# Performance work log

Hardware: AMD Instinct MI355X
Metric: run time of the kernel (lower is better)

Reference implementation:

```python
import jax, jax.numpy as jnp
import numpy as np

B, S, D, H = 2, 2048, 768, 12
DK = D // H

def setup_inputs() -> dict:
    key = jax.random.key(0)
    ks = jax.random.split(key, 8)
    query = jax.random.normal(ks[0], (B, S, D), dtype=jnp.float32)
    key_t = jax.random.normal(ks[1], (B, S, D), dtype=jnp.float32)
    value = jax.random.normal(ks[2], (B, S, D), dtype=jnp.float32)
    # causal (look-ahead) mask: True above the diagonal -> masked
    mask = jnp.triu(jnp.ones((S, S), dtype=bool), k=1)[None, None]  # (1,1,S,S)
    scale = 1.0 / np.sqrt(D)
    w_q = jax.random.normal(ks[3], (D, D), dtype=jnp.float32) * scale
    w_k = jax.random.normal(ks[4], (D, D), dtype=jnp.float32) * scale
    w_v = jax.random.normal(ks[5], (D, D), dtype=jnp.float32) * scale
    w_o = jax.random.normal(ks[6], (D, D), dtype=jnp.float32) * scale
    return {"query": query, "key": key_t, "value": value, "mask": mask,
            "w_q": w_q, "w_k": w_k, "w_v": w_v, "w_o": w_o}

def reference(query, key, value, mask, w_q, w_k, w_v, w_o):
    b = query.shape[0]
    # nn.Linear(bias=False): y = x @ W.T
    q = (query @ w_q.T).reshape(b, -1, H, DK).transpose(0, 2, 1, 3)  # (B,H,Sq,dk)
    k = (key @ w_k.T).reshape(b, -1, H, DK).transpose(0, 2, 1, 3)    # (B,H,Sk,dk)
    v = (value @ w_v.T).reshape(b, -1, H, DK).transpose(0, 2, 1, 3)  # (B,H,Sk,dk)
    scores = jnp.einsum('bhqd,bhkd->bhqk', q, k) / jnp.sqrt(jnp.float32(DK))
    scores = jnp.where(mask, jnp.float32(-1e9), scores)
    attn_weights = jax.nn.softmax(scores, axis=-1)  # (B,H,Sq,Sk); dropout=0 (eval)
    context = jnp.einsum('bhqk,bhkd->bhqd', attn_weights, v)
    context = context.transpose(0, 2, 1, 3).reshape(b, -1, D)
    output = context @ w_o.T
    return output, attn_weights
```

## Files before the change

### kernel.cpp

```cpp
#include <hip/hip_runtime.h>

#define BATCH 2
#define S_LEN 2048
#define NH 12
#define DMODEL 768

#define N8_BSD (BATCH * S_LEN * DMODEL / 8)
#define N8_DD (DMODEL * DMODEL / 8)

typedef __attribute__((ext_vector_type(8))) short bf16x8;
typedef __attribute__((ext_vector_type(4))) float f32x4;
typedef __attribute__((ext_vector_type(4))) unsigned short us4;

__device__ __forceinline__ unsigned short f2bf(float f) {
  union { float f; unsigned int u; } v; v.f = f;
  unsigned int r = v.u + 0x7fffu + ((v.u >> 16) & 1u);
  return (unsigned short)(r >> 16);
}

__global__ void cvt3_kernel(const float* __restrict__ s0,
                            const float* __restrict__ s1,
                            const float* __restrict__ s2,
                            unsigned short* __restrict__ dst,
                            float* __restrict__ ctx1) {
  int i = blockIdx.x * blockDim.x + threadIdx.x;
  int j = i / N8_BSD;
  int k = i - j * N8_BSD;
  const float* s = (j == 0) ? s0 : (j == 1) ? s1 : s2;
  const float4* sp = (const float4*)s;
  float4 a = sp[k * 2], b = sp[k * 2 + 1];
  us4 o0 = { f2bf(a.x), f2bf(a.y), f2bf(a.z), f2bf(a.w) };
  us4 o1 = { f2bf(b.x), f2bf(b.y), f2bf(b.z), f2bf(b.w) };
  us4* d = (us4*)dst;
  d[i * 2] = o0;
  d[i * 2 + 1] = o1;
  if (j == 0) {
    f32x4 z = (f32x4){0.f, 0.f, 0.f, 0.f};
    f32x4* c = (f32x4*)ctx1;
    c[k * 2] = z;
    c[k * 2 + 1] = z;
  }
}

__global__ void cvt4_kernel(const float* __restrict__ s0,
                            const float* __restrict__ s1,
                            const float* __restrict__ s2,
                            const float* __restrict__ s3,
                            unsigned short* __restrict__ dst) {
  int i = blockIdx.x * blockDim.x + threadIdx.x;
  int j = i / N8_DD;
  int k = i - j * N8_DD;
  const float* s = (j == 0) ? s0 : (j == 1) ? s1 : (j == 2) ? s2 : s3;
  const float4* sp = (const float4*)s;
  float4 a = sp[k * 2], b = sp[k * 2 + 1];
  us4 o0 = { f2bf(a.x), f2bf(a.y), f2bf(a.z), f2bf(a.w) };
  us4 o1 = { f2bf(b.x), f2bf(b.y), f2bf(b.z), f2bf(b.w) };
  us4* d = (us4*)dst;
  d[i * 2] = o0;
  d[i * 2 + 1] = o1;
}

__global__ void ctx_reduce(const float* __restrict__ c0,
                           const float* __restrict__ c1,
                           unsigned short* __restrict__ o) {
  int i = blockIdx.x * blockDim.x + threadIdx.x;
  float4 a = ((const float4*)c0)[i];
  float4 b = ((const float4*)c1)[i];
  us4 r = { f2bf(a.x + b.x), f2bf(a.y + b.y), f2bf(a.z + b.z), f2bf(a.w + b.w) };
  ((us4*)o)[i] = r;
}

#define GLD_LDS16(g, l)                                                    \
  __builtin_amdgcn_global_load_lds(                                        \
      (const __attribute__((address_space(1))) unsigned int*)(g),          \
      (__attribute__((address_space(3))) unsigned int*)(l), 16, 0, 0)

__global__ __launch_bounds__(256, 2)
void gemm_qkv(const unsigned short* __restrict__ Aq,
              const unsigned short* __restrict__ Ak,
              const unsigned short* __restrict__ Av,
              const unsigned short* __restrict__ W3,
              unsigned short* __restrict__ Qs,
              unsigned short* __restrict__ Ks,
              unsigned short* __restrict__ VT) {
  __shared__ unsigned short As[128 * 64];
  __shared__ unsigned short Bs[128 * 64];
  const int m0 = blockIdx.x * 128;
  const int n0g = blockIdx.y * 128;
  const int nblk = n0g / 768;
  const int n0 = n0g - nblk * 768;
  const unsigned short* A = (nblk == 0) ? Aq : (nblk == 1) ? Ak : Av;
  const unsigned short* Bw = W3 + (size_t)n0g * DMODEL;
  const int tid = threadIdx.x, w = tid >> 6, l = tid & 63;
  const int lg = l >> 4, ll = l & 15;
  const int wm = w >> 1, wn = w & 1;
  const int lr = l >> 3, lc = (l & 7) * 8;

  f32x4 acc[4][4];
#pragma unroll
  for (int i = 0; i < 4; ++i)
#pragma unroll
    for (int j = 0; j < 4; ++j) acc[i][j] = (f32x4){0.f, 0.f, 0.f, 0.f};

  for (int k0 = 0; k0 < DMODEL; k0 += 64) {
#pragma unroll
    for (int i = 0; i < 4; ++i) {
      GLD_LDS16(A + (size_t)(m0 + w * 32 + i * 8 + lr) * DMODEL + k0 + lc,
                &As[(w * 32 + i * 8) * 64]);
      GLD_LDS16(Bw + (size_t)(w * 32 + i * 8 + lr) * DMODEL + k0 + lc,
                &Bs[(w * 32 + i * 8) * 64]);
    }
    __syncthreads();
#pragma unroll
    for (int t = 0; t < 2; ++t) {
      bf16x8 af[4], bf[4];
#pragma unroll
      for (int mi = 0; mi < 4; ++mi)
        af[mi] = *(const bf16x8*)&As[(wm * 64 + mi * 16 + ll) * 64 + t * 32 + lg * 8];
#pragma unroll
      for (int ni = 0; ni < 4; ++ni)
        bf[ni] = *(const bf16x8*)&Bs[(wn * 64 + ni * 16 + ll) * 64 + t * 32 + lg * 8];
#pragma unroll
      for (int mi = 0; mi < 4; ++mi)
#pragma unroll
        for (int ni = 0; ni < 4; ++ni)
          acc[mi][ni] = __builtin_amdgcn_mfma_f32_16x16x32_bf16(
              af[mi], bf[ni], acc[mi][ni], 0, 0, 0);
    }
    __syncthreads();
  }

  if (nblk < 2) {
    unsigned short* o = nblk ? Ks : Qs;
    const float sc = nblk ? 1.f : 0.125f;
#pragma unroll
    for (int mi = 0; mi < 4; ++mi)
#pragma unroll
      for (int ni = 0; ni < 4; ++ni) {
        const int col = n0 + wn * 64 + ni * 16 + ll;
        const int rowb = m0 + wm * 64 + mi * 16 + lg * 4;
#pragma unroll
        for (int r = 0; r < 4; ++r)
          o[(size_t)(rowb + r) * 768 + col] = f2bf(acc[mi][ni][r] * sc);
      }
  } else {
#pragma unroll
    for (int mi = 0; mi < 4; ++mi)
#pragma unroll
      for (int ni = 0; ni < 4; ++ni) {
        const int col = n0 + wn * 64 + ni * 16 + ll;
        const int row = m0 + wm * 64 + mi * 16 + lg * 4;
        const int bb = row >> 11, sidx = row & (S_LEN - 1);
        const size_t base =
            ((size_t)(bb * NH + (col >> 6)) * 64 + (col & 63)) * S_LEN + sidx;
        us4 pk = { f2bf(acc[mi][ni][0]), f2bf(acc[mi][ni][1]),
                   f2bf(acc[mi][ni][2]), f2bf(acc[mi][ni][3]) };
        *(us4*)&VT[base] = pk;
      }
  }
}

__global__ __launch_bounds__(256, 2)
void gemm_proj(const unsigned short* __restrict__ A,
               const unsigned short* __restrict__ Bw,
               float* __restrict__ o) {
  __shared__ unsigned short As[128 * 64];
  __shared__ unsigned short Bs[128 * 64];
  const int m0 = blockIdx.x * 128, n0 = blockIdx.y * 128;
  const int tid = threadIdx.x, w = tid >> 6, l = tid & 63;
  const int lg = l >> 4, ll = l & 15;
  const int wm = w >> 1, wn = w & 1;
  const int lr = l >> 3, lc = (l & 7) * 8;

  f32x4 acc[4][4];
#pragma unroll
  for (int i = 0; i < 4; ++i)
#pragma unroll
    for (int j = 0; j < 4; ++j) acc[i][j] = (f32x4){0.f, 0.f, 0.f, 0.f};

  for (int k0 = 0; k0 < DMODEL; k0 += 64) {
#pragma unroll
    for (int i = 0; i < 4; ++i) {
      GLD_LDS16(A + (size_t)(m0 + w * 32 + i * 8 + lr) * DMODEL + k0 + lc,
                &As[(w * 32 + i * 8) * 64]);
      GLD_LDS16(Bw + (size_t)(n0 + w * 32 + i * 8 + lr) * DMODEL + k0 + lc,
                &Bs[(w * 32 + i * 8) * 64]);
    }
    __syncthreads();
#pragma unroll
    for (int t = 0; t < 2; ++t) {
      bf16x8 af[4], bf[4];
#pragma unroll
      for (int mi = 0; mi < 4; ++mi)
        af[mi] = *(const bf16x8*)&As[(wm * 64 + mi * 16 + ll) * 64 + t * 32 + lg * 8];
#pragma unroll
      for (int ni = 0; ni < 4; ++ni)
        bf[ni] = *(const bf16x8*)&Bs[(wn * 64 + ni * 16 + ll) * 64 + t * 32 + lg * 8];
#pragma unroll
      for (int mi = 0; mi < 4; ++mi)
#pragma unroll
        for (int ni = 0; ni < 4; ++ni)
          acc[mi][ni] = __builtin_amdgcn_mfma_f32_16x16x32_bf16(
              af[mi], bf[ni], acc[mi][ni], 0, 0, 0);
    }
    __syncthreads();
  }

#pragma unroll
  for (int mi = 0; mi < 4; ++mi)
#pragma unroll
    for (int ni = 0; ni < 4; ++ni) {
      const int col = n0 + wn * 64 + ni * 16 + ll;
      const int rowb = m0 + wm * 64 + mi * 16 + lg * 4;
#pragma unroll
      for (int r = 0; r < 4; ++r)
        o[(size_t)(rowb + r) * DMODEL + col] = acc[mi][ni][r];
    }
}

#define STAGE_TILE(srcTile, srcStride, ldsT)                                  \
  {                                                                           \
    _Pragma("unroll") for (int j_ = 0; j_ < 2; ++j_) {                        \
      int slot_ = (j_ * 4 + w) * 64 + l;                                      \
      int row_ = slot_ >> 3, c16_ = slot_ & 7;                                \
      GLD_LDS16((srcTile) + (size_t)row_ * (srcStride) +                      \
                    ((c16_ ^ (row_ & 7)) << 3),                               \
                (ldsT) + (j_ * 4 + w) * 512);                                 \
    }                                                                         \
  }

__global__ __launch_bounds__(256, 3)
void attn_ml(const unsigned short* __restrict__ Qp,
             const unsigned short* __restrict__ Kp,
             float2* __restrict__ mlbuf) {
  const int idx = blockIdx.x;
  const int qt = 31 - idx / (NH * BATCH);
  const int hb = idx % (NH * BATCH);
  const int h = hb >> 1, b = hb & 1;
  const int tid = threadIdx.x, w = tid >> 6, l = tid & 63;
  const int lg = l >> 4, ll = l & 15;
  __shared__ unsigned short Kt[2][64 * 64];

  const unsigned short* kbp = Kp + (size_t)b * S_LEN * DMODEL + h * 64;
  const int q0 = qt * 64 + w * 16;
  const int nkt = qt + 1;

  bf16x8 qf[2];
  {
    const unsigned short* qb =
        Qp + (size_t)(b * S_LEN + q0 + ll) * DMODEL + h * 64 + lg * 8;
    qf[0] = *(const bf16x8*)qb;
    qf[1] = *(const bf16x8*)(qb + 32);
  }
  int rowg[4];
#pragma unroll
  for (int r = 0; r < 4; ++r) rowg[r] = q0 + lg * 4 + r;

  float m[4], lsum[4];
#pragma unroll
  for (int r = 0; r < 4; ++r) { m[r] = -1e30f; lsum[r] = 0.f; }

  STAGE_TILE(kbp + (size_t)0 * 64 * DMODEL, DMODEL, &Kt[0][0]);
  __syncthreads();

  for (int kt = 0; kt < nkt; ++kt) {
    const int cur = kt & 1;
    if (kt + 1 < nkt)
      STAGE_TILE(kbp + (size_t)(kt + 1) * 64 * DMODEL, DMODEL, &Kt[cur ^ 1][0]);
    bf16x8 kf[8];
#pragma unroll
    for (int t = 0; t < 2; ++t)
#pragma unroll
      for (int nb = 0; nb < 4; ++nb) {
        const int row = nb * 16 + ll;
        kf[t * 4 + nb] = *(const bf16x8*)&Kt[cur][row * 64 +
            (((t * 4 + lg) ^ (row & 7)) << 3)];
      }
    f32x4 sv[4];
#pragma unroll
    for (int nb = 0; nb < 4; ++nb) sv[nb] = (f32x4){0.f, 0.f, 0.f, 0.f};
#pragma unroll
    for (int t = 0; t < 2; ++t)
#pragma unroll
      for (int nb = 0; nb < 4; ++nb)
        sv[nb] = __builtin_amdgcn_mfma_f32_16x16x32_bf16(qf[t], kf[t * 4 + nb],
                                                         sv[nb], 0, 0, 0);
    if (kt == nkt - 1) {
#pragma unroll
      for (int nb = 0; nb < 4; ++nb) {
        const int col = kt * 64 + nb * 16 + ll;
#pragma unroll
        for (int r = 0; r < 4; ++r)
          if (col > rowg[r]) sv[nb][r] = -1e30f;
      }
    }
#pragma unroll
    for (int r = 0; r < 4; ++r) {
      float tm = fmaxf(fmaxf(sv[0][r], sv[1][r]), fmaxf(sv[2][r], sv[3][r]));
      float mn = fmaxf(m[r], tm);
      float te = __expf(sv[0][r] - mn) + __expf(sv[1][r] - mn) +
                 __expf(sv[2][r] - mn) + __expf(sv[3][r] - mn);
      lsum[r] = lsum[r] * __expf(m[r] - mn) + te;
      m[r] = mn;
    }
    __syncthreads();
  }

#pragma unroll
  for (int off = 1; off < 16; off <<= 1)
#pragma unroll
    for (int r = 0; r < 4; ++r) {
      float om = __shfl_xor(m[r], off, 64);
      float ol = __shfl_xor(lsum[r], off, 64);
      float mn = fmaxf(m[r], om);
      lsum[r] = lsum[r] * __expf(m[r] - mn) + ol * __expf(om - mn);
      m[r] = mn;
    }

  if (ll == 0) {
    float2* mlb = mlbuf + (size_t)(b * NH + h) * S_LEN;
#pragma unroll
    for (int r = 0; r < 4; ++r)
      mlb[rowg[r]] = make_float2(m[r], 1.f / lsum[r]);
  }
}

__global__ __launch_bounds__(256, 3)
void attn_p2(const unsigned short* __restrict__ Qp,
             const unsigned short* __restrict__ Kp,
             const unsigned short* __restrict__ VTp,
             const float2* __restrict__ mlbuf,
             float* __restrict__ attnw,
             float* __restrict__ ctx0,
             float* __restrict__ ctx1) {
  const int idx = blockIdx.x;
  const int slot = idx / (NH * BATCH);
  const int hb = idx % (NH * BATCH);
  const int h = hb >> 1, b = hb & 1;
  int qt, ck;
  if (slot <= 16)      { ck = 0; qt = 15 + slot; }
  else if (slot == 17) { ck = 1; qt = 31; }
  else if (slot < 48)  { int u = slot - 18; int k = 15 - (u >> 1);
                         if (u & 1) { ck = 1; qt = k + 15; } else { ck = 0; qt = k - 1; } }
  else                 { ck = 1; qt = slot - 48; }

  const int ktlo = ck * 16;
  const int kthi = (qt < ktlo + 15) ? qt : (ktlo + 15);
  const bool hasval = (ktlo <= qt);

  const int tid = threadIdx.x, w = tid >> 6, l = tid & 63;
  const int lg = l >> 4, ll = l & 15;
  __shared__ unsigned short Kt[2][64 * 64];
  __shared__ unsigned short Vt[2][64 * 64];
  __shared__ float pf32[4][1024];
  float* pfw = &pf32[w][0];

  const unsigned short* kbp = Kp + (size_t)b * S_LEN * DMODEL + h * 64;
  const unsigned short* vbp = VTp + ((size_t)(b * NH + h)) * 64 * S_LEN;
  float* pbase = attnw + ((size_t)(b * NH + h)) * S_LEN * S_LEN;

  const int q0 = qt * 64 + w * 16;
  int rowg[4];
#pragma unroll
  for (int r = 0; r < 4; ++r) rowg[r] = q0 + lg * 4 + r;

  if (hasval) {
    bf16x8 qf[2];
    {
      const unsigned short* qb =
          Qp + (size_t)(b * S_LEN + q0 + ll) * DMODEL + h * 64 + lg * 8;
      qf[0] = *(const bf16x8*)qb;
      qf[1] = *(const bf16x8*)(qb + 32);
    }
    float m[4], linv[4];
    {
      const float2* mlb = mlbuf + (size_t)(b * NH + h) * S_LEN;
#pragma unroll
      for (int r = 0; r < 4; ++r) {
        float2 t = mlb[rowg[r]];
        m[r] = t.x;
        linv[r] = t.y;
      }
    }

    f32x4 cacc[4];
#pragma unroll
    for (int nb = 0; nb < 4; ++nb) cacc[nb] = (f32x4){0.f, 0.f, 0.f, 0.f};

    STAGE_TILE(kbp + (size_t)ktlo * 64 * DMODEL, DMODEL, &Kt[0][0]);
    STAGE_TILE(vbp + (size_t)ktlo * 64, S_LEN, &Vt[0][0]);
    __syncthreads();

    for (int kt = ktlo; kt <= kthi; ++kt) {
      const int cur = (kt - ktlo) & 1;
      if (kt < kthi) {
        STAGE_TILE(kbp + (size_t)(kt + 1) * 64 * DMODEL, DMODEL, &Kt[cur ^ 1][0]);
        STAGE_TILE(vbp + (size_t)(kt + 1) * 64, S_LEN, &Vt[cur ^ 1][0]);
      }
      bf16x8 kf[8];
#pragma unroll
      for (int t = 0; t < 2; ++t)
#pragma unroll
        for (int nb = 0; nb < 4; ++nb) {
          const int row = nb * 16 + ll;
          kf[t * 4 + nb] = *(const bf16x8*)&Kt[cur][row * 64 +
              (((t * 4 + lg) ^ (row & 7)) << 3)];
        }
      f32x4 sv[4];
#pragma unroll
      for (int nb = 0; nb < 4; ++nb) sv[nb] = (f32x4){0.f, 0.f, 0.f, 0.f};
#pragma unroll
      for (int t = 0; t < 2; ++t)
#pragma unroll
        for (int nb = 0; nb < 4; ++nb)
          sv[nb] = __builtin_amdgcn_mfma_f32_16x16x32_bf16(qf[t], kf[t * 4 + nb],
                                                           sv[nb], 0, 0, 0);
#pragma unroll
      for (int nb = 0; nb < 4; ++nb) {
        const int col = kt * 64 + nb * 16 + ll;
#pragma unroll
        for (int r = 0; r < 4; ++r) {
          float p = (col <= rowg[r]) ? __expf(sv[nb][r] - m[r]) * linv[r] : 0.f;
          const int rl = lg * 4 + r;
          pfw[rl * 64 + ((nb * 16 + ll) ^ ((lg & 1) << 4))] = p;
        }
      }
      bf16x8 pf[2];
#pragma unroll
      for (int t = 0; t < 2; ++t) {
        const int c0 = (t * 32 + lg * 8) ^ (((ll >> 2) & 1) << 4);
        f32x4 lo = *(const f32x4*)&pfw[ll * 64 + c0];
        f32x4 hi = *(const f32x4*)&pfw[ll * 64 + c0 + 4];
        union { us4 hh[2]; bf16x8 v; } u;
        u.hh[0] = (us4){ f2bf(lo[0]), f2bf(lo[1]), f2bf(lo[2]), f2bf(lo[3]) };
        u.hh[1] = (us4){ f2bf(hi[0]), f2bf(hi[1]), f2bf(hi[2]), f2bf(hi[3]) };
        pf[t] = u.v;
      }
      bf16x8 vf[8];
#pragma unroll
      for (int t = 0; t < 2; ++t)
#pragma unroll
        for (int nb = 0; nb < 4; ++nb) {
          const int row = nb * 16 + ll;
          vf[t * 4 + nb] = *(const bf16x8*)&Vt[cur][row * 64 +
              (((t * 4 + lg) ^ (row & 7)) << 3)];
        }
#pragma unroll
      for (int t = 0; t < 2; ++t)
#pragma unroll
        for (int nb = 0; nb < 4; ++nb)
          cacc[nb] = __builtin_amdgcn_mfma_f32_16x16x32_bf16(
              pf[t], vf[t * 4 + nb], cacc[nb], 0, 0, 0);
#pragma unroll
      for (int ps = 0; ps < 4; ++ps) {
        const int row = ps * 4 + lg;
        const int cb = (ll * 4) ^ ((ps & 1) << 4);
        f32x4 pv = *(const f32x4*)&pfw[row * 64 + cb];
        *(f32x4*)&pbase[(size_t)(q0 + row) * S_LEN + kt * 64 + ll * 4] = pv;
      }
      __syncthreads();
    }

#pragma unroll
    for (int nb = 0; nb < 4; ++nb)
#pragma unroll
      for (int r = 0; r < 4; ++r) {
        const int rl = lg * 4 + r;
        pfw[rl * 64 + ((nb * 16 + ll) ^ ((lg & 1) << 4))] = cacc[nb][r];
      }
    float* co = ck ? ctx1 : ctx0;
#pragma unroll
    for (int ps = 0; ps < 4; ++ps) {
      const int row = ps * 4 + lg;
      const int cb = (ll * 4) ^ ((ps & 1) << 4);
      f32x4 cv = *(const f32x4*)&pfw[row * 64 + cb];
      *(f32x4*)&co[(size_t)(b * S_LEN + q0 + row) * DMODEL + h * 64 + ll * 4] = cv;
    }
  }

  const int zs = ((qt + 1) * 64 > ktlo * 64) ? (qt + 1) * 64 : ktlo * 64;
  const int ze = (ktlo + 16) * 64;
  if (zs < ze) {
    f32x4 z = (f32x4){0.f, 0.f, 0.f, 0.f};
    for (int rr = 0; rr < 16; ++rr) {
      float* dst = pbase + (size_t)(q0 + rr) * S_LEN;
      for (int c = zs + l * 4; c < ze; c += 256)
        *(f32x4*)(dst + c) = z;
    }
  }
}

extern "C" void kernel_launch(void* const* d_in, const int* in_sizes, int n_in,
                              void* d_out, int out_size, void* d_ws, size_t ws_size,
                              hipStream_t stream) {
  const float* q_in = (const float*)d_in[0];
  const float* k_in = (const float*)d_in[1];
  const float* v_in = (const float*)d_in[2];
  const float* wq = (const float*)d_in[4];
  const float* wk = (const float*)d_in[5];
  const float* wv = (const float*)d_in[6];
  const float* wo = (const float*)d_in[7];

  const int BSD = BATCH * S_LEN * DMODEL;
  const int DD = DMODEL * DMODEL;
  const int M = BATCH * S_LEN;

  char* ws = (char*)d_ws;
  unsigned short* qbf = (unsigned short*)ws;  ws += (size_t)BSD * 2;
  unsigned short* kbf = (unsigned short*)ws;  ws += (size_t)BSD * 2;
  unsigned short* vbf = (unsigned short*)ws;  ws += (size_t)BSD * 2;
  unsigned short* wqb = (unsigned short*)ws;  ws += (size_t)DD * 2;
  unsigned short* wkb = (unsigned short*)ws;  ws += (size_t)DD * 2;
  unsigned short* wvb = (unsigned short*)ws;  ws += (size_t)DD * 2;
  unsigned short* wob = (unsigned short*)ws;  ws += (size_t)DD * 2;
  unsigned short* Qs  = (unsigned short*)ws;  ws += (size_t)BSD * 2;
  unsigned short* Ks  = (unsigned short*)ws;  ws += (size_t)BSD * 2;
  unsigned short* VT  = (unsigned short*)ws;  ws += (size_t)BSD * 2;
  unsigned short* ctx = (unsigned short*)ws;  ws += (size_t)BSD * 2;
  float* ctx0 = (float*)ws;                   ws += (size_t)BSD * 4;
  float* ctx1 = (float*)ws;                   ws += (size_t)BSD * 4;
  float2* mlbuf = (float2*)ws;                ws += (size_t)M * NH * sizeof(float2);
  (void)wkb; (void)wvb;

  float* out_proj = (float*)d_out;
  float* attnw = (float*)d_out + BSD;

  cvt3_kernel<<<3 * N8_BSD / 256, 256, 0, stream>>>(q_in, k_in, v_in, qbf, ctx1);
  cvt4_kernel<<<4 * N8_DD / 256, 256, 0, stream>>>(wq, wk, wv, wo, wqb);

  gemm_qkv<<<dim3(M / 128, 2304 / 128), 256, 0, stream>>>(qbf, kbf, vbf, wqb,
                                                          Qs, Ks, VT);

  attn_ml<<<32 * NH * BATCH, 256, 0, stream>>>(Qs, Ks, mlbuf);
  attn_p2<<<64 * NH * BATCH, 256, 0, stream>>>(Qs, Ks, VT, mlbuf, attnw,
                                               ctx0, ctx1);
  ctx_reduce<<<BSD / 4 / 256, 256, 0, stream>>>(ctx0, ctx1, ctx);

  gemm_proj<<<dim3(M / 128, DMODEL / 128), 256, 0, stream>>>(ctx, wob, out_proj);
}
```

Measured before the change: 218.4 us.

## Split attention pass-2 key tiles across warps with LDS cross-warp context reduction

Each warp now handles all 64 query rows of the tile for every fourth key tile, instead of each warp owning 16 query rows across all key tiles. K and V fragments are read straight from global memory rather than double-buffered through shared memory, which removes the per-tile __syncthreads. The four per-warp partial contexts are summed through shared memory at the end. This costs more registers (occupancy hint drops from 3 to 2), a larger per-warp LDS scratch, and uncached, uncoalesced-style global K/V reads. Blocks with few key tiles also leave some warps idle.

```diff
diff --git a/kernel.cpp b/kernel.cpp
--- a/kernel.cpp
+++ b/kernel.cpp
@@ -325,7 +325,7 @@
   }
 }
 
-__global__ __launch_bounds__(256, 3)
+__global__ __launch_bounds__(256, 2)
 void attn_p2(const unsigned short* __restrict__ Qp,
              const unsigned short* __restrict__ Kp,
              const unsigned short* __restrict__ VTp,
@@ -350,140 +350,149 @@
 
   const int tid = threadIdx.x, w = tid >> 6, l = tid & 63;
   const int lg = l >> 4, ll = l & 15;
-  __shared__ unsigned short Kt[2][64 * 64];
-  __shared__ unsigned short Vt[2][64 * 64];
-  __shared__ float pf32[4][1024];
+  __shared__ float pf32[4][64 * 64];
   float* pfw = &pf32[w][0];
 
   const unsigned short* kbp = Kp + (size_t)b * S_LEN * DMODEL + h * 64;
   const unsigned short* vbp = VTp + ((size_t)(b * NH + h)) * 64 * S_LEN;
   float* pbase = attnw + ((size_t)(b * NH + h)) * S_LEN * S_LEN;
-
-  const int q0 = qt * 64 + w * 16;
-  int rowg[4];
-#pragma unroll
-  for (int r = 0; r < 4; ++r) rowg[r] = q0 + lg * 4 + r;
+  const int q0g = qt * 64;
 
   if (hasval) {
-    bf16x8 qf[2];
-    {
+    bf16x8 qf[4][2];
+#pragma unroll
+    for (int rb = 0; rb < 4; ++rb) {
       const unsigned short* qb =
-          Qp + (size_t)(b * S_LEN + q0 + ll) * DMODEL + h * 64 + lg * 8;
-      qf[0] = *(const bf16x8*)qb;
-      qf[1] = *(const bf16x8*)(qb + 32);
-    }
-    float m[4], linv[4];
+          Qp + (size_t)(b * S_LEN + q0g + rb * 16 + ll) * DMODEL + h * 64 + lg * 8;
+      qf[rb][0] = *(const bf16x8*)qb;
+      qf[rb][1] = *(const bf16x8*)(qb + 32);
+    }
+    float m16[4][4], li16[4][4];
     {
       const float2* mlb = mlbuf + (size_t)(b * NH + h) * S_LEN;
 #pragma unroll
-      for (int r = 0; r < 4; ++r) {
-        float2 t = mlb[rowg[r]];
-        m[r] = t.x;
-        linv[r] = t.y;
-      }
-    }
-
-    f32x4 cacc[4];
-#pragma unroll
-    for (int nb = 0; nb < 4; ++nb) cacc[nb] = (f32x4){0.f, 0.f, 0.f, 0.f};
-
-    STAGE_TILE(kbp + (size_t)ktlo * 64 * DMODEL, DMODEL, &Kt[0][0]);
-    STAGE_TILE(vbp + (size_t)ktlo * 64, S_LEN, &Vt[0][0]);
-    __syncthreads();
-
-    for (int kt = ktlo; kt <= kthi; ++kt) {
-      const int cur = (kt - ktlo) & 1;
-      if (kt < kthi) {
-        STAGE_TILE(kbp + (size_t)(kt + 1) * 64 * DMODEL, DMODEL, &Kt[cur ^ 1][0]);
-        STAGE_TILE(vbp + (size_t)(kt + 1) * 64, S_LEN, &Vt[cur ^ 1][0]);
-      }
-      bf16x8 kf[8];
-#pragma unroll
-      for (int t = 0; t < 2; ++t)
-#pragma unroll
-        for (int nb = 0; nb < 4; ++nb) {
-          const int row = nb * 16 + ll;
-          kf[t * 4 + nb] = *(const bf16x8*)&Kt[cur][row * 64 +
-              (((t * 4 + lg) ^ (row & 7)) << 3)];
+      for (int rb = 0; rb < 4; ++rb)
+#pragma unroll
+        for (int r = 0; r < 4; ++r) {
+          float2 t = mlb[q0g + rb * 16 + lg * 4 + r];
+          m16[rb][r] = t.x;
+          li16[rb][r] = t.y;
         }
-      f32x4 sv[4];
-#pragma unroll
-      for (int nb = 0; nb < 4; ++nb) sv[nb] = (f32x4){0.f, 0.f, 0.f, 0.f};
-#pragma unroll
-      for (int t = 0; t < 2; ++t)
-#pragma unroll
-        for (int nb = 0; nb < 4; ++nb)
-          sv[nb] = __builtin_amdgcn_mfma_f32_16x16x32_bf16(qf[t], kf[t * 4 + nb],
-                                                           sv[nb], 0, 0, 0);
-#pragma unroll
-      for (int nb = 0; nb < 4; ++nb) {
-        const int col = kt * 64 + nb * 16 + ll;
-#pragma unroll
-        for (int r = 0; r < 4; ++r) {
-          float p = (col <= rowg[r]) ? __expf(sv[nb][r] - m[r]) * linv[r] : 0.f;
-          const int rl = lg * 4 + r;
-          pfw[rl * 64 + ((nb * 16 + ll) ^ ((lg & 1) << 4))] = p;
+    }
+
+    f32x4 cacc[4][4];
+#pragma unroll
+    for (int rb = 0; rb < 4; ++rb)
+#pragma unroll
+      for (int vb = 0; vb < 4; ++vb) cacc[rb][vb] = (f32x4){0.f, 0.f, 0.f, 0.f};
+
+    for (int kt = ktlo + w; kt <= kthi; kt += 4) {
+#pragma unroll
+      for (int hh = 0; hh < 2; ++hh) {
+        bf16x8 kf[2][2];
+#pragma unroll
+        for (int t = 0; t < 2; ++t)
+#pragma unroll
+          for (int nbl = 0; nbl < 2; ++nbl) {
+            const int nb = hh * 2 + nbl;
+            kf[t][nbl] = *(const bf16x8*)(kbp +
+                (size_t)(kt * 64 + nb * 16 + ll) * DMODEL + t * 32 + lg * 8);
+          }
+        f32x4 sv[4][2];
+#pragma unroll
+        for (int rb = 0; rb < 4; ++rb)
+#pragma unroll
+          for (int nbl = 0; nbl < 2; ++nbl) sv[rb][nbl] = (f32x4){0.f, 0.f, 0.f, 0.f};
+#pragma unroll
+        for (int t = 0; t < 2; ++t)
+#pragma unroll
+          for (int rb = 0; rb < 4; ++rb)
+#pragma unroll
+            for (int nbl = 0; nbl < 2; ++nbl)
+              sv[rb][nbl] = __builtin_amdgcn_mfma_f32_16x16x32_bf16(
+                  qf[rb][t], kf[t][nbl], sv[rb][nbl], 0, 0, 0);
+#pragma unroll
+        for (int nbl = 0; nbl < 2; ++nbl) {
+          const int nb = hh * 2 + nbl;
+          const int col = kt * 64 + nb * 16 + ll;
+#pragma unroll
+          for (int rb = 0; rb < 4; ++rb)
+#pragma unroll
+            for (int r = 0; r < 4; ++r) {
+              const int row = q0g + rb * 16 + lg * 4 + r;
+              float p = (col <= row)
+                            ? __expf(sv[rb][nbl][r] - m16[rb][r]) * li16[rb][r]
+                            : 0.f;
+              pfw[(rb * 16 + lg * 4 + r) * 64 +
+                  ((nb * 16 + ll) ^ ((lg & 1) << 4))] = p;
+            }
         }
       }
-      bf16x8 pf[2];
 #pragma unroll
       for (int t = 0; t < 2; ++t) {
-        const int c0 = (t * 32 + lg * 8) ^ (((ll >> 2) & 1) << 4);
-        f32x4 lo = *(const f32x4*)&pfw[ll * 64 + c0];
-        f32x4 hi = *(const f32x4*)&pfw[ll * 64 + c0 + 4];
-        union { us4 hh[2]; bf16x8 v; } u;
-        u.hh[0] = (us4){ f2bf(lo[0]), f2bf(lo[1]), f2bf(lo[2]), f2bf(lo[3]) };
-        u.hh[1] = (us4){ f2bf(hi[0]), f2bf(hi[1]), f2bf(hi[2]), f2bf(hi[3]) };
-        pf[t] = u.v;
-      }
-      bf16x8 vf[8];
-#pragma unroll
-      for (int t = 0; t < 2; ++t)
-#pragma unroll
-        for (int nb = 0; nb < 4; ++nb) {
-          const int row = nb * 16 + ll;
-          vf[t * 4 + nb] = *(const bf16x8*)&Vt[cur][row * 64 +
-              (((t * 4 + lg) ^ (row & 7)) << 3)];
+        bf16x8 pfr[4];
+#pragma unroll
+        for (int rb = 0; rb < 4; ++rb) {
+          const int row = rb * 16 + ll;
+          const int c0 = (t * 32 + lg * 8) ^ (((ll >> 2) & 1) << 4);
+          f32x4 lo = *(const f32x4*)&pfw[row * 64 + c0];
+          f32x4 hi = *(const f32x4*)&pfw[row * 64 + c0 + 4];
+          union { us4 hh2[2]; bf16x8 v; } u;
+          u.hh2[0] = (us4){ f2bf(lo[0]), f2bf(lo[1]), f2bf(lo[2]), f2bf(lo[3]) };
+          u.hh2[1] = (us4){ f2bf(hi[0]), f2bf(hi[1]), f2bf(hi[2]), f2bf(hi[3]) };
+          pfr[rb] = u.v;
         }
-#pragma unroll
-      for (int t = 0; t < 2; ++t)
-#pragma unroll
-        for (int nb = 0; nb < 4; ++nb)
-          cacc[nb] = __builtin_amdgcn_mfma_f32_16x16x32_bf16(
-              pf[t], vf[t * 4 + nb], cacc[nb], 0, 0, 0);
-#pragma unroll
-      for (int ps = 0; ps < 4; ++ps) {
+        bf16x8 vf[4];
+#pragma unroll
+        for (int vb = 0; vb < 4; ++vb)
+          vf[vb] = *(const bf16x8*)(vbp +
+              (size_t)(vb * 16 + ll) * S_LEN + kt * 64 + t * 32 + lg * 8);
+#pragma unroll
+        for (int rb = 0; rb < 4; ++rb)
+#pragma unroll
+          for (int vb = 0; vb < 4; ++vb)
+            cacc[rb][vb] = __builtin_amdgcn_mfma_f32_16x16x32_bf16(
+                pfr[rb], vf[vb], cacc[rb][vb], 0, 0, 0);
+      }
+#pragma unroll
+      for (int ps = 0; ps < 16; ++ps) {
         const int row = ps * 4 + lg;
         const int cb = (ll * 4) ^ ((ps & 1) << 4);
         f32x4 pv = *(const f32x4*)&pfw[row * 64 + cb];
-        *(f32x4*)&pbase[(size_t)(q0 + row) * S_LEN + kt * 64 + ll * 4] = pv;
-      }
-      __syncthreads();
-    }
-
-#pragma unroll
-    for (int nb = 0; nb < 4; ++nb)
-#pragma unroll
-      for (int r = 0; r < 4; ++r) {
-        const int rl = lg * 4 + r;
-        pfw[rl * 64 + ((nb * 16 + ll) ^ ((lg & 1) << 4))] = cacc[nb][r];
-      }
+        *(f32x4*)&pbase[(size_t)(q0g + row) * S_LEN + kt * 64 + ll * 4] = pv;
+      }
+    }
+
+#pragma unroll
+    for (int rb = 0; rb < 4; ++rb)
+#pragma unroll
+      for (int vb = 0; vb < 4; ++vb)
+#pragma unroll
+        for (int r = 0; r < 4; ++r)
+          pfw[(rb * 16 + lg * 4 + r) * 64 +
+              ((vb * 16 + ll) ^ ((lg & 1) << 4))] = cacc[rb][vb][r];
+    __syncthreads();
     float* co = ck ? ctx1 : ctx0;
 #pragma unroll
-    for (int ps = 0; ps < 4; ++ps) {
-      const int row = ps * 4 + lg;
-      const int cb = (ll * 4) ^ ((ps & 1) << 4);
-      f32x4 cv = *(const f32x4*)&pfw[row * 64 + cb];
-      *(f32x4*)&co[(size_t)(b * S_LEN + q0 + row) * DMODEL + h * 64 + ll * 4] = cv;
-    }
-  }
-
+    for (int ps2 = 0; ps2 < 4; ++ps2) {
+      const int row = w * 16 + ps2 * 4 + lg;
+      const int cb = (ll * 4) ^ ((ps2 & 1) << 4);
+      f32x4 s0 = *(const f32x4*)&pf32[0][row * 64 + cb];
+      f32x4 s1 = *(const f32x4*)&pf32[1][row * 64 + cb];
+      f32x4 s2 = *(const f32x4*)&pf32[2][row * 64 + cb];
+      f32x4 s3 = *(const f32x4*)&pf32[3][row * 64 + cb];
+      f32x4 sm = (s0 + s1) + (s2 + s3);
+      *(f32x4*)&co[(size_t)(b * S_LEN + q0g + row) * DMODEL + h * 64 + ll * 4] = sm;
+    }
+  }
+
+  const int q0w = qt * 64 + w * 16;
   const int zs = ((qt + 1) * 64 > ktlo * 64) ? (qt + 1) * 64 : ktlo * 64;
   const int ze = (ktlo + 16) * 64;
   if (zs < ze) {
     f32x4 z = (f32x4){0.f, 0.f, 0.f, 0.f};
     for (int rr = 0; rr < 16; ++rr) {
-      float* dst = pbase + (size_t)(q0 + rr) * S_LEN;
+      float* dst = pbase + (size_t)(q0w + rr) * S_LEN;
       for (int c = zs + l * 4; c < ze; c += 256)
         *(f32x4*)(dst + c) = z;
     }
```

Result: no change. 214.5 us (-1.8%).
